# Kernel optimization log

Measured on AMD Instinct MI355X. Metric: run time of the kernel, lower is better.

Reference implementation:

```python
import jax, jax.numpy as jnp
import numpy as np

MODES = 2
LC = 4
N = 6000
KNN = 10
NODES = 64
CH = MODES ** 2
M = N * 2 * (KNN + 1)  # total candidate couplings


def setup_inputs() -> dict:
    key = jax.random.key(0)
    ks = jax.random.split(key, 6)
    return {
        "CK_inputs": jax.random.normal(ks[0], (N, 2 * (KNN + 1), 3), dtype=jnp.float32),
        "W_in": jax.random.normal(ks[1], (3, NODES), dtype=jnp.float32) * 0.1,
        "b_in": jnp.zeros((NODES,), dtype=jnp.float32),
        "W_hid": jax.random.normal(ks[2], (LC - 1, NODES, NODES), dtype=jnp.float32) * 0.1,
        "b_hid": jnp.zeros((LC - 1, NODES), dtype=jnp.float32),
        "W_out": jax.random.normal(ks[3], (NODES, CH), dtype=jnp.float32) * 0.1,
        "b_out": jnp.zeros((CH,), dtype=jnp.float32),
        "coo": jax.random.randint(ks[4], (2, M), 0, N, dtype=jnp.int32),
    }


def _mlp(x, W_in, b_in, W_hid, b_hid, W_out, b_out):
    # MLP: 3 -> 64, (LC-1) hidden 64->64 layers, 64 -> CH; ReLU activations.
    h = jax.nn.relu(x @ W_in + b_in)
    for i in range(W_hid.shape[0]):  # small fixed layer count
        h = jax.nn.relu(h @ W_hid[i] + b_hid[i])
    return h @ W_out + b_out  # [M, CH]


def reference(CK_inputs, W_in, b_in, W_hid, b_hid, W_out, b_out, coo):
    C_stripped = _mlp(CK_inputs.reshape(-1, 3), W_in, b_in, W_hid, b_hid, W_out, b_out)  # [M, CH]
    D = MODES * N
    # Original: for channel ch = mi*MODES+mj, scatter C_stripped[:, ch] at indices coo*MODES+mj
    # (mj added to BOTH row and col, replicating the source exactly). Indices are
    # independent of mi, so sum over mi first, then one scatter-add per mj.
    vals = C_stripped.reshape(-1, MODES, MODES).sum(axis=1)  # [M, MODES]; axis1=mi, axis2=mj
    dense = jnp.zeros((D, D), dtype=CK_inputs.dtype)
    for mj in range(MODES):
        idx = coo * MODES + mj  # [2, M]
        dense = dense.at[idx[0], idx[1]].add(vals[:, mj])
    return dense
```

## Files before the change

kernel.cpp:

```cpp
#include <hip/hip_runtime.h>
#include <stdint.h>

#define NN    6000
#define KNNC  10
#define MM    (NN * 2 * (KNNC + 1))
#define DD    (2 * NN)
#define LCH   3
#define BLK   256

#define NV          ((long long)DD * DD / 4)
#define FILL_BLOCKS 4096
#define MLP_BLOCKS  ((MM + BLK - 1) / BLK)

__global__ __launch_bounds__(BLK) void fill_out(float* __restrict__ out) {
    float4 z = make_float4(0.f, 0.f, 0.f, 0.f);
    float4* outv = (float4*)out;
    long long i = (long long)blockIdx.x * BLK + threadIdx.x;
    const long long stride = (long long)FILL_BLOCKS * BLK;
    for (; i < NV; i += stride) outv[i] = z;
}

__global__ __launch_bounds__(BLK) void mlp(
    const float* __restrict__ CK,
    const float* __restrict__ Win,
    const float* __restrict__ bin,
    const float* __restrict__ Whid,
    const float* __restrict__ bhid,
    const float* __restrict__ Wout,
    const float* __restrict__ bout,
    float* __restrict__ vals)
{
    const int m = blockIdx.x * BLK + threadIdx.x;
    if (m >= MM) return;

    const float x0 = CK[m * 3 + 0];
    const float x1 = CK[m * 3 + 1];
    const float x2 = CK[m * 3 + 2];

    float h[64];
#pragma unroll
    for (int j = 0; j < 64; j++) {
        float a = bin[j];
        a = fmaf(x0, Win[j],       a);
        a = fmaf(x1, Win[64 + j],  a);
        a = fmaf(x2, Win[128 + j], a);
        h[j] = fmaxf(a, 0.0f);
    }

#pragma unroll 1
    for (int l = 0; l < LCH; l++) {
        const float4* __restrict__ W4 = (const float4*)(Whid + (l << 12));
        const float*  __restrict__ bh = bhid + (l << 6);
        float g[64];
#pragma unroll
        for (int j = 0; j < 64; j++) g[j] = bh[j];
#pragma unroll 2
        for (int k = 0; k < 64; k++) {
            const float hk = h[k];
            const float4* __restrict__ Wk = W4 + (k << 4);
#pragma unroll
            for (int j4 = 0; j4 < 16; j4++) {
                float4 w = Wk[j4];
                g[j4 * 4 + 0] = fmaf(w.x, hk, g[j4 * 4 + 0]);
                g[j4 * 4 + 1] = fmaf(w.y, hk, g[j4 * 4 + 1]);
                g[j4 * 4 + 2] = fmaf(w.z, hk, g[j4 * 4 + 2]);
                g[j4 * 4 + 3] = fmaf(w.w, hk, g[j4 * 4 + 3]);
            }
        }
#pragma unroll
        for (int j = 0; j < 64; j++) h[j] = fmaxf(g[j], 0.0f);
    }

    float v0 = bout[0] + bout[2];
    float v1 = bout[1] + bout[3];
#pragma unroll
    for (int k = 0; k < 64; k++) {
        float4 wo = *((const float4*)Wout + k);
        v0 = fmaf(h[k], wo.x + wo.z, v0);
        v1 = fmaf(h[k], wo.y + wo.w, v1);
    }
    vals[m * 2 + 0] = v0;
    vals[m * 2 + 1] = v1;
}

__global__ __launch_bounds__(BLK) void scatter_add(
    const float* __restrict__ vals,
    const int* __restrict__ coo,
    float* __restrict__ out)
{
    const int t = blockIdx.x * BLK + threadIdx.x;
    if (t >= MM) return;
    const int r2 = coo[t] * 2;
    const int c2 = coo[MM + t] * 2;
    const float v0 = vals[t * 2 + 0];
    const float v1 = vals[t * 2 + 1];
    const long long f0 = (long long)r2 * DD + c2;
    atomicAdd(out + f0, v0);
    atomicAdd(out + f0 + DD + 1, v1);
}

extern "C" void kernel_launch(void* const* d_in, const int* in_sizes, int n_in,
                              void* d_out, int out_size, void* d_ws, size_t ws_size,
                              hipStream_t stream) {
    const float* CK   = (const float*)d_in[0];
    const float* Win  = (const float*)d_in[1];
    const float* bin  = (const float*)d_in[2];
    const float* Whid = (const float*)d_in[3];
    const float* bhid = (const float*)d_in[4];
    const float* Wout = (const float*)d_in[5];
    const float* bout = (const float*)d_in[6];
    const int* coo    = (const int*)d_in[7];
    float* out        = (float*)d_out;
    float* vals       = (float*)d_ws;

    fill_out<<<FILL_BLOCKS, BLK, 0, stream>>>(out);
    mlp<<<MLP_BLOCKS, BLK, 0, stream>>>(CK, Win, bin, Whid, bhid, Wout, bout, vals);
    scatter_add<<<MLP_BLOCKS, BLK, 0, stream>>>(vals, coo, out);
}
```

Measured before the change: 746.6 us.

## Fuse MLP and scatter into lane-per-neuron persistent kernel with register-resident weights

Replaces the thread-per-sample MLP with a persistent kernel in which each wave handles four samples at a time. Each lane owns one output neuron, keeps its column of all three hidden weight matrices in registers, and broadcasts activations across the wave with readlane. The output layer is reduced with cross-lane shuffles and the results are scatter-added straight into the output, which removes the intermediate vals buffer and the separate scatter launch. The cost is a large register footprint (192 weight floats per lane), which limits occupancy, plus extra readlane and shuffle instructions. The fill of the dense 12000x12000 output, roughly 576 MB, is unchanged and likely dominates total time.

```diff
diff --git a/kernel.cpp b/kernel.cpp
--- a/kernel.cpp
+++ b/kernel.cpp
@@ -5,12 +5,13 @@
 #define KNNC  10
 #define MM    (NN * 2 * (KNNC + 1))
 #define DD    (2 * NN)
-#define LCH   3
 #define BLK   256
 
 #define NV          ((long long)DD * DD / 4)
 #define FILL_BLOCKS 4096
-#define MLP_BLOCKS  ((MM + BLK - 1) / BLK)
+#define MLP_BLOCKS  512
+#define NWAVES      (MLP_BLOCKS * 4)
+#define NGRP        ((MM + 3) / 4)
 
 __global__ __launch_bounds__(BLK) void fill_out(float* __restrict__ out) {
     float4 z = make_float4(0.f, 0.f, 0.f, 0.f);
@@ -20,7 +21,12 @@
     for (; i < NV; i += stride) outv[i] = z;
 }
 
-__global__ __launch_bounds__(BLK) void mlp(
+__device__ __forceinline__ float rlane(float v, int l) {
+    return __builtin_bit_cast(float,
+        __builtin_amdgcn_readlane(__builtin_bit_cast(int, v), l));
+}
+
+__global__ __launch_bounds__(BLK, 2) void mlp_scatter(
     const float* __restrict__ CK,
     const float* __restrict__ Win,
     const float* __restrict__ bin,
@@ -28,75 +34,94 @@
     const float* __restrict__ bhid,
     const float* __restrict__ Wout,
     const float* __restrict__ bout,
-    float* __restrict__ vals)
+    const int*   __restrict__ coo,
+    float* __restrict__ out)
 {
-    const int m = blockIdx.x * BLK + threadIdx.x;
-    if (m >= MM) return;
+    const int tid  = threadIdx.x;
+    const int lane = tid & 63;
+    const int gwid = blockIdx.x * 4 + (tid >> 6);
 
-    const float x0 = CK[m * 3 + 0];
-    const float x1 = CK[m * 3 + 1];
-    const float x2 = CK[m * 3 + 2];
+    float W0[64], W1[64], W2[64];
+#pragma unroll
+    for (int k = 0; k < 64; k++) W0[k] = Whid[k * 64 + lane];
+#pragma unroll
+    for (int k = 0; k < 64; k++) W1[k] = Whid[4096 + k * 64 + lane];
+#pragma unroll
+    for (int k = 0; k < 64; k++) W2[k] = Whid[8192 + k * 64 + lane];
 
-    float h[64];
-#pragma unroll
-    for (int j = 0; j < 64; j++) {
-        float a = bin[j];
-        a = fmaf(x0, Win[j],       a);
-        a = fmaf(x1, Win[64 + j],  a);
-        a = fmaf(x2, Win[128 + j], a);
-        h[j] = fmaxf(a, 0.0f);
+    const float wi0 = Win[lane], wi1 = Win[64 + lane], wi2 = Win[128 + lane];
+    const float b0  = bin[lane];
+    const float bh0 = bhid[lane], bh1 = bhid[64 + lane], bh2 = bhid[128 + lane];
+    const float4 wo = ((const float4*)Wout)[lane];
+    const float wc0 = wo.x + wo.z;
+    const float wc1 = wo.y + wo.w;
+    const float bo0 = bout[0] + bout[2];
+    const float bo1 = bout[1] + bout[3];
+
+#define HIDDEN(W, BH)                                                   \
+    {                                                                   \
+        float g0 = (BH), g1 = (BH), g2 = (BH), g3 = (BH);               \
+        _Pragma("unroll")                                               \
+        for (int k = 0; k < 64; k++) {                                  \
+            g0 = fmaf(W[k], rlane(h0, k), g0);                          \
+            g1 = fmaf(W[k], rlane(h1, k), g1);                          \
+            g2 = fmaf(W[k], rlane(h2, k), g2);                          \
+            g3 = fmaf(W[k], rlane(h3, k), g3);                          \
+        }                                                               \
+        h0 = fmaxf(g0, 0.f); h1 = fmaxf(g1, 0.f);                       \
+        h2 = fmaxf(g2, 0.f); h3 = fmaxf(g3, 0.f);                       \
     }
 
-#pragma unroll 1
-    for (int l = 0; l < LCH; l++) {
-        const float4* __restrict__ W4 = (const float4*)(Whid + (l << 12));
-        const float*  __restrict__ bh = bhid + (l << 6);
-        float g[64];
+    for (int grp = gwid; grp < NGRP; grp += NWAVES) {
+        const int rowbase = grp * 4;
+
+        float vck = 0.f;
+        const int cidx = rowbase * 3 + lane;
+        if (lane < 12 && cidx < MM * 3) vck = CK[cidx];
+
+        float h0 = fmaxf(fmaf(rlane(vck, 2), wi2,
+                         fmaf(rlane(vck, 1), wi1,
+                         fmaf(rlane(vck, 0), wi0, b0))), 0.f);
+        float h1 = fmaxf(fmaf(rlane(vck, 5), wi2,
+                         fmaf(rlane(vck, 4), wi1,
+                         fmaf(rlane(vck, 3), wi0, b0))), 0.f);
+        float h2 = fmaxf(fmaf(rlane(vck, 8), wi2,
+                         fmaf(rlane(vck, 7), wi1,
+                         fmaf(rlane(vck, 6), wi0, b0))), 0.f);
+        float h3 = fmaxf(fmaf(rlane(vck, 11), wi2,
+                         fmaf(rlane(vck, 10), wi1,
+                         fmaf(rlane(vck, 9), wi0, b0))), 0.f);
+
+        HIDDEN(W0, bh0)
+        HIDDEN(W1, bh1)
+        HIDDEN(W2, bh2)
+
+        float p00 = h0 * wc0, p01 = h0 * wc1;
+        float p10 = h1 * wc0, p11 = h1 * wc1;
+        float p20 = h2 * wc0, p21 = h2 * wc1;
+        float p30 = h3 * wc0, p31 = h3 * wc1;
 #pragma unroll
-        for (int j = 0; j < 64; j++) g[j] = bh[j];
-#pragma unroll 2
-        for (int k = 0; k < 64; k++) {
-            const float hk = h[k];
-            const float4* __restrict__ Wk = W4 + (k << 4);
-#pragma unroll
-            for (int j4 = 0; j4 < 16; j4++) {
-                float4 w = Wk[j4];
-                g[j4 * 4 + 0] = fmaf(w.x, hk, g[j4 * 4 + 0]);
-                g[j4 * 4 + 1] = fmaf(w.y, hk, g[j4 * 4 + 1]);
-                g[j4 * 4 + 2] = fmaf(w.z, hk, g[j4 * 4 + 2]);
-                g[j4 * 4 + 3] = fmaf(w.w, hk, g[j4 * 4 + 3]);
-            }
+        for (int m = 32; m; m >>= 1) {
+            p00 += __shfl_xor(p00, m, 64);  p01 += __shfl_xor(p01, m, 64);
+            p10 += __shfl_xor(p10, m, 64);  p11 += __shfl_xor(p11, m, 64);
+            p20 += __shfl_xor(p20, m, 64);  p21 += __shfl_xor(p21, m, 64);
+            p30 += __shfl_xor(p30, m, 64);  p31 += __shfl_xor(p31, m, 64);
         }
-#pragma unroll
-        for (int j = 0; j < 64; j++) h[j] = fmaxf(g[j], 0.0f);
+
+        float a0 = lane == 0 ? p00 : lane == 1 ? p10 : lane == 2 ? p20 : p30;
+        float a1 = lane == 0 ? p01 : lane == 1 ? p11 : lane == 2 ? p21 : p31;
+        a0 += bo0;
+        a1 += bo1;
+        const int myrow = rowbase + lane;
+        if (lane < 4 && myrow < MM) {
+            const int r2 = coo[myrow] * 2;
+            const int c2 = coo[MM + myrow] * 2;
+            const long long f0 = (long long)r2 * DD + c2;
+            atomicAdd(out + f0, a0);
+            atomicAdd(out + f0 + DD + 1, a1);
+        }
     }
-
-    float v0 = bout[0] + bout[2];
-    float v1 = bout[1] + bout[3];
-#pragma unroll
-    for (int k = 0; k < 64; k++) {
-        float4 wo = *((const float4*)Wout + k);
-        v0 = fmaf(h[k], wo.x + wo.z, v0);
-        v1 = fmaf(h[k], wo.y + wo.w, v1);
-    }
-    vals[m * 2 + 0] = v0;
-    vals[m * 2 + 1] = v1;
-}
-
-__global__ __launch_bounds__(BLK) void scatter_add(
-    const float* __restrict__ vals,
-    const int* __restrict__ coo,
-    float* __restrict__ out)
-{
-    const int t = blockIdx.x * BLK + threadIdx.x;
-    if (t >= MM) return;
-    const int r2 = coo[t] * 2;
-    const int c2 = coo[MM + t] * 2;
-    const float v0 = vals[t * 2 + 0];
-    const float v1 = vals[t * 2 + 1];
-    const long long f0 = (long long)r2 * DD + c2;
-    atomicAdd(out + f0, v0);
-    atomicAdd(out + f0 + DD + 1, v1);
+#undef HIDDEN
 }
 
 extern "C" void kernel_launch(void* const* d_in, const int* in_sizes, int n_in,
@@ -111,9 +136,8 @@
     const float* bout = (const float*)d_in[6];
     const int* coo    = (const int*)d_in[7];
     float* out        = (float*)d_out;
-    float* vals       = (float*)d_ws;
 
     fill_out<<<FILL_BLOCKS, BLK, 0, stream>>>(out);
-    mlp<<<MLP_BLOCKS, BLK, 0, stream>>>(CK, Win, bin, Whid, bhid, Wout, bout, vals);
-    scatter_add<<<MLP_BLOCKS, BLK, 0, stream>>>(vals, coo, out);
+    mlp_scatter<<<MLP_BLOCKS, BLK, 0, stream>>>(
+        CK, Win, bin, Whid, bhid, Wout, bout, coo, out);
 }
```

Result: no change. 736.8 us (-1.3%).
